# Kernel tuning notes

Measured on AMD Instinct MI355X. Metric: run time of the kernel, lower is better.

Reference implementation:

```python
import jax, jax.numpy as jnp
import numpy as np
import math

S, B, F, D, H, L, DFF, PRED = 448, 64, 8, 256, 8, 4, 256, 96
DK = D // H
EPS = 1e-5


def _pos_enc(length, d_model):
    pos = jnp.arange(length, dtype=jnp.float32)[:, None]            # [S,1]
    div = jnp.exp(jnp.arange(0, d_model, 2, dtype=jnp.float32) * (-math.log(10000.0) / d_model))
    pe = jnp.zeros((length, d_model), jnp.float32)
    pe = pe.at[:, 0::2].set(jnp.sin(pos * div))
    pe = pe.at[:, 1::2].set(jnp.cos(pos * div))
    return pe[:, None, :]                                            # [S,1,D]


def _layernorm(x, g, b):
    mu = jnp.mean(x, axis=-1, keepdims=True)
    var = jnp.mean((x - mu) ** 2, axis=-1, keepdims=True)
    return (x - mu) / jnp.sqrt(var + EPS) * g + b


def setup_inputs() -> dict:
    key = jax.random.key(0)
    ks = jax.random.split(key, 12)
    g = lambda k, shape: (jax.random.normal(k, shape) * 0.02).astype(jnp.float32)
    return {
        "src": jax.random.normal(ks[0], (S, B, F), jnp.float32),
        "w_in": g(ks[1], (F, D)), "b_in": jnp.zeros((D,), jnp.float32),
        "Wq": g(ks[2], (L, D, D)), "bq": jnp.zeros((L, D), jnp.float32),
        "Wk": g(ks[3], (L, D, D)), "bk": jnp.zeros((L, D), jnp.float32),
        "Wv": g(ks[4], (L, D, D)), "bv": jnp.zeros((L, D), jnp.float32),
        "Wo": g(ks[5], (L, D, D)), "bo": jnp.zeros((L, D), jnp.float32),
        "g1": jnp.ones((L, D), jnp.float32), "be1": jnp.zeros((L, D), jnp.float32),
        "W1": g(ks[6], (L, D, DFF)), "b1": jnp.zeros((L, DFF), jnp.float32),
        "W2": g(ks[7], (L, DFF, D)), "b2": jnp.zeros((L, D), jnp.float32),
        "g2": jnp.ones((L, D), jnp.float32), "be2": jnp.zeros((L, D), jnp.float32),
        "w_out": g(ks[8], (D, F)), "b_out": jnp.zeros((F,), jnp.float32),
    }


def reference(src, w_in, b_in, Wq, bq, Wk, bk, Wv, bv, Wo, bo,
              g1, be1, W1, b1, W2, b2, g2, be2, w_out, b_out):
    x = src @ w_in + b_in                 # [S,B,D]
    x = x + _pos_enc(S, D)

    scale = math.sqrt(DK)

    def layer(x, p):
        wq, bq_, wk, bk_, wv, bv_, wo, bo_, g1_, be1_, w1, b1_, w2, b2_, g2_, be2_ = p
        Q = (x @ wq + bq_).reshape(S, B, H, DK)
        K = (x @ wk + bk_).reshape(S, B, H, DK)
        V = (x @ wv + bv_).reshape(S, B, H, DK)
        scores = jnp.einsum("sbhd,tbhd->bhst", Q, K) / scale   # [B,H,S,S]
        attn = jax.nn.softmax(scores, axis=-1)
        ctx = jnp.einsum("bhst,tbhd->sbhd", attn, V).reshape(S, B, D)
        x = _layernorm(x + (ctx @ wo + bo_), g1_, be1_)
        ff = jax.nn.relu(x @ w1 + b1_) @ w2 + b2_
        x = _layernorm(x + ff, g2_, be2_)
        return x, None

    x, _ = jax.lax.scan(layer, x, (Wq, bq, Wk, bk, Wv, bv, Wo, bo,
                                   g1, be1, W1, b1, W2, b2, g2, be2))
    return x[-PRED:] @ w_out + b_out      # [PRED,B,F]
```

## Files before the change

### kernel.cpp

```cpp
#include <hip/hip_runtime.h>
#include <hip/hip_bf16.h>
#include <math.h>

#define S_ 448
#define B_ 64
#define F_ 8
#define D_ 256
#define H_ 8
#define DK_ 32
#define L_ 4
#define PRED_ 96
#define NT_ (S_ * B_)
#define PANEL_ (S_ * DK_)
#define VTP_ (32 * 512)

typedef unsigned short bf16_t;
using bf16x8 = __attribute__((ext_vector_type(8))) short;
using f32x4  = __attribute__((ext_vector_type(4))) float;
using f32x16 = __attribute__((ext_vector_type(16))) float;

__device__ __forceinline__ float b2f(bf16_t b) {
  return __uint_as_float(((unsigned)b) << 16);
}
__device__ __forceinline__ bf16_t f2b(float f) {
  unsigned u = __float_as_uint(f);
  u += 0x7fffu + ((u >> 16) & 1u);
  return (bf16_t)(u >> 16);
}
__device__ __forceinline__ unsigned pk2(float lo, float hi) {
  union { __hip_bfloat162 h; unsigned u; } c;
  c.h = __float22bfloat162_rn(make_float2(lo, hi));
  return c.u;
}

__global__ __launch_bounds__(256) void embed_kernel(
    const float* __restrict__ src, const float* __restrict__ w_in,
    const float* __restrict__ b_in, bf16_t* __restrict__ x) {
  int n = blockIdx.x;
  int d = threadIdx.x;
  const float* srow = src + (size_t)n * F_;
  float acc = b_in[d];
#pragma unroll
  for (int f = 0; f < F_; ++f) acc += srow[f] * w_in[f * D_ + d];
  int s = n / B_;
  int i2 = d & ~1;
  float freq = __expf(-9.210340371976184f * (float)i2 / (float)D_);
  float ang = (float)s * freq;
  float pe = (d & 1) ? cosf(ang) : sinf(ang);
  x[(size_t)n * D_ + d] = f2b(acc + pe);
}

__global__ __launch_bounds__(256) void transpose_w_kernel(
    const float* __restrict__ W, bf16_t* __restrict__ Wt) {
  __shared__ float t[32][33];
  int l = blockIdx.z;
  int k0 = blockIdx.x * 32, n0 = blockIdx.y * 32;
  int x = threadIdx.x, y = threadIdx.y;
  const float* src = W + ((size_t)l * 256 + k0) * 256 + n0;
#pragma unroll
  for (int i = y; i < 32; i += 8) t[i][x] = src[(size_t)i * 256 + x];
  __syncthreads();
  bf16_t* dst = Wt + ((size_t)l * 256 + n0) * 256 + k0;
#pragma unroll
  for (int i = y; i < 32; i += 8) dst[(size_t)i * 256 + x] = f2b(t[x][i]);
}

__global__ __launch_bounds__(512) void vtrans_kernel(
    const bf16_t* __restrict__ V, bf16_t* __restrict__ Vt) {
  __shared__ bf16_t t[32][456];
  int bh = blockIdx.x, tid = threadIdx.x;
  const bf16_t* Vp = V + (size_t)bh * PANEL_;
#pragma unroll
  for (int p = 0; p < 4; ++p) {
    int idx = tid + p * 512;
    if (idx < 1792) {
      int s = idx >> 2, c = idx & 3;
      uint4 v = *(const uint4*)(Vp + s * 32 + c * 8);
      unsigned w[4] = {v.x, v.y, v.z, v.w};
#pragma unroll
      for (int e = 0; e < 8; ++e) {
        bf16_t val = (bf16_t)((e & 1) ? (w[e >> 1] >> 16) : (w[e >> 1] & 0xffff));
        *(bf16_t*)((char*)&t[0][0] + (c * 8 + e) * 912 + s * 2) = val;
      }
    }
  }
  __syncthreads();
  bf16_t* Op = Vt + (size_t)bh * VTP_;
#pragma unroll
  for (int p = 0; p < 4; ++p) {
    int idx = tid + p * 512;
    int dk = idx >> 6, sl = idx & 63;
    uint4 v = {0, 0, 0, 0};
    if (sl < 56) v = *(const uint4*)((char*)&t[0][0] + dk * 912 + sl * 16);
    *(uint4*)(Op + dk * 512 + sl * 8) = v;
  }
}

template <int ALAY, int OLAY, int RELU>
__device__ __forceinline__ void gemm_body(
    const bf16_t* __restrict__ A, const bf16_t* __restrict__ Wt,
    const float* __restrict__ bias, bf16_t* __restrict__ Y, int m0, int n0) {
  __shared__ bf16_t As[2][128][32];
  __shared__ bf16_t Bs[2][128][32];
  int tid = threadIdx.x, lane = tid & 63, wv = tid >> 6;
  int wr = wv >> 2, wc = wv & 3;
  int jg = lane >> 4, fr = lane & 15;
  int s_row = tid >> 2;
  int s_p = tid & 3;

  uint4 rA, rB;

  auto stage_load = [&](int kt) {
    int k0 = kt * 32;
    int ls = s_p ^ ((s_row >> 1) & 3);
    const bf16_t* ap;
    if (ALAY == 0) {
      ap = A + (size_t)(m0 + s_row) * 256 + k0 + ls * 8;
    } else {
      int n = m0 + s_row;
      int k = k0 + ls * 8;
      ap = A + ((size_t)(((n & 63) << 3) | (k >> 5)) * S_ + (n >> 6)) * DK_ +
           (k & 31);
    }
    rA = *(const uint4*)ap;
    rB = *(const uint4*)(Wt + (size_t)(n0 + s_row) * 256 + k0 + ls * 8);
  };
  auto stage_write = [&](int buf) {
    *(uint4*)(&As[buf][s_row][s_p * 8]) = rA;
    *(uint4*)(&Bs[buf][s_row][s_p * 8]) = rB;
  };

  f32x4 zero = {0.f, 0.f, 0.f, 0.f};
  f32x4 acc[4][2];
#pragma unroll
  for (int i = 0; i < 4; ++i)
#pragma unroll
    for (int j = 0; j < 2; ++j) acc[i][j] = zero;

  stage_load(0);
  stage_write(0);
  __syncthreads();

  for (int kt = 0; kt < 8; ++kt) {
    int buf = kt & 1;
    if (kt < 7) stage_load(kt + 1);
    bf16x8 af[4], bfr[2];
#pragma unroll
    for (int mi = 0; mi < 4; ++mi) {
      int row = wr * 64 + mi * 16 + fr;
      af[mi] = *(const bf16x8*)((const char*)&As[buf][0][0] + row * 64 +
                                ((jg ^ ((row >> 1) & 3)) << 4));
    }
#pragma unroll
    for (int ni = 0; ni < 2; ++ni) {
      int rn = wc * 32 + ni * 16 + fr;
      bfr[ni] = *(const bf16x8*)((const char*)&Bs[buf][0][0] + rn * 64 +
                                 ((jg ^ ((rn >> 1) & 3)) << 4));
    }
#pragma unroll
    for (int mi = 0; mi < 4; ++mi)
#pragma unroll
      for (int ni = 0; ni < 2; ++ni)
        acc[mi][ni] = __builtin_amdgcn_mfma_f32_16x16x32_bf16(
            af[mi], bfr[ni], acc[mi][ni], 0, 0, 0);
    if (kt < 7) {
      stage_write((kt + 1) & 1);
      __syncthreads();
    }
  }

  __syncthreads();
  char* ep0 = (char*)&As[0][0][0] + wv * 1024;
  float bcol[2];
#pragma unroll
  for (int ni = 0; ni < 2; ++ni) bcol[ni] = bias[n0 + wc * 32 + ni * 16 + fr];
#pragma unroll
  for (int mi = 0; mi < 4; ++mi) {
    char* ep = ep0 + (mi & 1) * 8192;
#pragma unroll
    for (int ni = 0; ni < 2; ++ni)
#pragma unroll
      for (int r = 0; r < 4; ++r) {
        float v = acc[mi][ni][r] + bcol[ni];
        if (RELU) v = fmaxf(v, 0.f);
        int row = jg * 4 + r;
        int cb = (ni * 16 + fr) * 2;
        *(bf16_t*)(ep + row * 64 + (cb ^ (jg << 4))) = f2b(v);
      }
    int row16 = lane >> 2, c = lane & 3;
    uint4 v = *(uint4*)(ep + row16 * 64 +
                        ((c << 4) ^ (((row16 >> 2) & 3) << 4)));
    int n = m0 + wr * 64 + mi * 16 + row16;
    if (OLAY == 0) {
      *(uint4*)((char*)(Y + (size_t)n * 256 + n0 + wc * 32) + c * 16) = v;
    } else {
      int h = (n0 + wc * 32) >> 5;
      *(uint4*)((char*)(Y + ((size_t)(((n & 63) << 3) | h) * S_ + (n >> 6)) *
                                DK_) +
                c * 16) = v;
    }
  }
}

__global__ __launch_bounds__(512, 4) void gemm_qkv_kernel(
    const bf16_t* __restrict__ A, const bf16_t* __restrict__ wq,
    const bf16_t* __restrict__ wk, const bf16_t* __restrict__ wvp,
    const float* __restrict__ bq, const float* __restrict__ bk,
    const float* __restrict__ bvp, bf16_t* __restrict__ yq,
    bf16_t* __restrict__ yk, bf16_t* __restrict__ yv) {
  int bid = blockIdx.x;
  int w = (bid & 7) * 168 + (bid >> 3);
  int sel = w % 6;
  int m0 = (w / 6) * 128;
  int mtx = sel >> 1;
  const bf16_t* W = mtx == 0 ? wq : mtx == 1 ? wk : wvp;
  const float* bb = mtx == 0 ? bq : mtx == 1 ? bk : bvp;
  bf16_t* Y = mtx == 0 ? yq : mtx == 1 ? yk : yv;
  gemm_body<0, 1, 0>(A, W, bb, Y, m0, (sel & 1) * 128);
}

__global__ __launch_bounds__(512, 4) void gemm_relu_kernel(
    const bf16_t* __restrict__ A, const bf16_t* __restrict__ Wt,
    const float* __restrict__ bias, bf16_t* __restrict__ Y) {
  int bid = blockIdx.x;
  int w = (bid & 7) * 56 + (bid >> 3);
  gemm_body<0, 0, 1>(A, Wt, bias, Y, (w >> 1) * 128, (w & 1) * 128);
}

template <int ALAY>
__global__ __launch_bounds__(512, 2) void gemm_ln_kernel(
    const bf16_t* __restrict__ A, const bf16_t* __restrict__ Wt,
    const float* __restrict__ bias, const float* __restrict__ g,
    const float* __restrict__ be, bf16_t* __restrict__ x) {
  __shared__ char smem[40960];
  int tid = threadIdx.x, lane = tid & 63, wv = tid >> 6;
  int wr = wv >> 2, wc = wv & 3;
  int jg = lane >> 4, fr = lane & 15;
  int bid = blockIdx.x;
  int m0 = ((bid & 7) * 56 + (bid >> 3)) * 64;

  uint4 rA, rB0, rB1;
  auto stage_load = [&](int kt) {
    int k0 = kt * 32;
    if (tid < 256) {
      int row = tid >> 2, p = tid & 3;
      int ls = p ^ ((row >> 1) & 3);
      const bf16_t* ap;
      if (ALAY == 0) {
        ap = A + (size_t)(m0 + row) * 256 + k0 + ls * 8;
      } else {
        int n = m0 + row;
        int k = k0 + ls * 8;
        ap = A + ((size_t)(((n & 63) << 3) | (k >> 5)) * S_ + (n >> 6)) * DK_ +
             (k & 31);
      }
      rA = *(const uint4*)ap;
    }
    int p = tid & 3;
    int r0 = tid >> 2, r1 = 128 + (tid >> 2);
    rB0 = *(const uint4*)(Wt + (size_t)r0 * 256 + k0 + (p ^ ((r0 >> 1) & 3)) * 8);
    rB1 = *(const uint4*)(Wt + (size_t)r1 * 256 + k0 + (p ^ ((r1 >> 1) & 3)) * 8);
  };
  auto stage_write = [&](int buf) {
    if (tid < 256)
      *(uint4*)(smem + buf * 4096 + (tid >> 2) * 64 + (tid & 3) * 16) = rA;
    char* bb = smem + 8192 + buf * 16384;
    *(uint4*)(bb + (tid >> 2) * 64 + (tid & 3) * 16) = rB0;
    *(uint4*)(bb + (128 + (tid >> 2)) * 64 + (tid & 3) * 16) = rB1;
  };

  f32x4 zero = {0.f, 0.f, 0.f, 0.f};
  f32x4 acc[2][4];
#pragma unroll
  for (int i = 0; i < 2; ++i)
#pragma unroll
    for (int j = 0; j < 4; ++j) acc[i][j] = zero;

  stage_load(0);
  stage_write(0);
  __syncthreads();

  for (int kt = 0; kt < 8; ++kt) {
    int buf = kt & 1;
    if (kt < 7) stage_load(kt + 1);
    bf16x8 af[2], bfr[4];
#pragma unroll
    for (int mi = 0; mi < 2; ++mi) {
      int row = wr * 32 + mi * 16 + fr;
      af[mi] = *(const bf16x8*)(smem + buf * 4096 + row * 64 +
                                ((jg ^ ((row >> 1) & 3)) << 4));
    }
#pragma unroll
    for (int ni = 0; ni < 4; ++ni) {
      int rn = wc * 64 + ni * 16 + fr;
      bfr[ni] = *(const bf16x8*)(smem + 8192 + buf * 16384 + rn * 64 +
                                 ((jg ^ ((rn >> 1) & 3)) << 4));
    }
#pragma unroll
    for (int mi = 0; mi < 2; ++mi)
#pragma unroll
      for (int ni = 0; ni < 4; ++ni)
        acc[mi][ni] = __builtin_amdgcn_mfma_f32_16x16x32_bf16(
            af[mi], bfr[ni], acc[mi][ni], 0, 0, 0);
    if (kt < 7) {
      stage_write((kt + 1) & 1);
      __syncthreads();
    }
  }

  __syncthreads();
  float* ssum = (float*)smem;
  float* ssq  = (float*)(smem + 1024);
  float* rowm = (float*)(smem + 2048);
  float* rowr = (float*)(smem + 2304);

  float bcol[4], gv[4], bev[4];
#pragma unroll
  for (int ni = 0; ni < 4; ++ni) {
    int c = wc * 64 + ni * 16 + fr;
    bcol[ni] = bias[c];
    gv[ni] = g[c];
    bev[ni] = be[c];
  }
#pragma unroll
  for (int mi = 0; mi < 2; ++mi)
#pragma unroll
    for (int r = 0; r < 4; ++r) {
      int row = wr * 32 + mi * 16 + jg * 4 + r;
      size_t gbase = (size_t)(m0 + row) * 256 + wc * 64 + fr;
      float s = 0.f, s2 = 0.f;
#pragma unroll
      for (int ni = 0; ni < 4; ++ni) {
        float v = acc[mi][ni][r] + bcol[ni] + b2f(x[gbase + ni * 16]);
        acc[mi][ni][r] = v;
        s += v;
        s2 += v * v;
      }
#pragma unroll
      for (int off = 1; off <= 8; off <<= 1) {
        s += __shfl_xor(s, off);
        s2 += __shfl_xor(s2, off);
      }
      if (fr == 0) {
        ssum[row * 4 + wc] = s;
        ssq[row * 4 + wc] = s2;
      }
    }
  __syncthreads();
  if (tid < 64) {
    float s = ssum[tid * 4] + ssum[tid * 4 + 1] + ssum[tid * 4 + 2] +
              ssum[tid * 4 + 3];
    float q = ssq[tid * 4] + ssq[tid * 4 + 1] + ssq[tid * 4 + 2] +
              ssq[tid * 4 + 3];
    float mean = s * (1.f / 256.f);
    float var = q * (1.f / 256.f) - mean * mean;
    rowm[tid] = mean;
    rowr[tid] = rsqrtf(var + 1e-5f);
  }
  __syncthreads();
  char* ep0 = smem + 8192 + wv * 2048;
#pragma unroll
  for (int mi = 0; mi < 2; ++mi) {
    char* ep = ep0 + mi * 16384;
#pragma unroll
    for (int r = 0; r < 4; ++r) {
      int row = wr * 32 + mi * 16 + jg * 4 + r;
      float mean = rowm[row], rinv = rowr[row];
#pragma unroll
      for (int ni = 0; ni < 4; ++ni) {
        float lnv = (acc[mi][ni][r] - mean) * rinv * gv[ni] + bev[ni];
        int cb = (ni * 16 + fr) * 2;
        *(bf16_t*)(ep + (jg * 4 + r) * 128 + (cb ^ (jg << 4))) = f2b(lnv);
      }
    }
    int row16 = lane >> 2;
#pragma unroll
    for (int ps = 0; ps < 2; ++ps) {
      int ch = (lane & 3) + ps * 4;
      uint4 v = *(uint4*)(ep + row16 * 128 + ((ch * 16) ^ ((row16 >> 2) << 4)));
      *(uint4*)(x + (size_t)(m0 + wr * 32 + mi * 16 + row16) * 256 + wc * 64 +
                ch * 8) = v;
    }
  }
}

__global__ __launch_bounds__(448) void attn_v5_kernel(
    bf16_t* __restrict__ Q, const bf16_t* __restrict__ K,
    const bf16_t* __restrict__ Vt) {
  __shared__ char Ep[7][2560];
  int tid = threadIdx.x, lane = tid & 63, wv = tid >> 6;
  int bid = blockIdx.x;
  int xcd = bid & 7, j = bid >> 3;
  int bh = ((j >> 1) << 3) | xcd;
  int qt = (j & 1) * 7 + wv;
  int q0 = qt * 32;
  bf16_t* Qp = Q + (size_t)bh * PANEL_;
  const bf16_t* Kp = K + (size_t)bh * PANEL_;
  const bf16_t* Vp = Vt + (size_t)bh * VTP_;
  int lo31 = lane & 31, hi = lane >> 5;
  const float sc_c = 0.25503484f;
  const f32x16 z16 = {0.f, 0.f, 0.f, 0.f, 0.f, 0.f, 0.f, 0.f,
                      0.f, 0.f, 0.f, 0.f, 0.f, 0.f, 0.f, 0.f};

  bf16x8 qf0 = *(const bf16x8*)(Qp + (q0 + lo31) * 32 + hi * 8);
  bf16x8 qf1 = *(const bf16x8*)(Qp + (q0 + lo31) * 32 + 16 + hi * 8);

  float m_run = -3.0e38f, l_run = 0.f;
  f32x16 o = z16;

  for (int kc = 0; kc < 7; ++kc) {
    int t0 = kc * 64;
    f32x16 s0 = z16, s1 = z16;
    {
      const bf16_t* kr0 = Kp + (t0 + lo31) * 32 + hi * 8;
      const bf16_t* kr1 = Kp + (t0 + 32 + lo31) * 32 + hi * 8;
      bf16x8 ka0 = *(const bf16x8*)(kr0);
      bf16x8 ka1 = *(const bf16x8*)(kr0 + 16);
      bf16x8 kb0 = *(const bf16x8*)(kr1);
      bf16x8 kb1 = *(const bf16x8*)(kr1 + 16);
      __builtin_amdgcn_s_setprio(1);
      s0 = __builtin_amdgcn_mfma_f32_32x32x16_bf16(ka0, qf0, s0, 0, 0, 0);
      s0 = __builtin_amdgcn_mfma_f32_32x32x16_bf16(ka1, qf1, s0, 0, 0, 0);
      s1 = __builtin_amdgcn_mfma_f32_32x32x16_bf16(kb0, qf0, s1, 0, 0, 0);
      s1 = __builtin_amdgcn_mfma_f32_32x32x16_bf16(kb1, qf1, s1, 0, 0, 0);
      __builtin_amdgcn_s_setprio(0);
    }
    float cm = -3.0e38f;
#pragma unroll
    for (int r = 0; r < 16; ++r) cm = fmaxf(cm, fmaxf(s0[r], s1[r]));
    cm = fmaxf(cm, __shfl_xor(cm, 32));
    if (!__all(cm <= m_run + 16.0f)) {
      float m_new = fmaxf(m_run, cm);
      float scale = exp2f((m_run - m_new) * sc_c);
      l_run *= scale;
#pragma unroll
      for (int r = 0; r < 16; ++r) o[r] *= scale;
      m_run = m_new;
    }
    float ls = 0.f;
#pragma unroll
    for (int r = 0; r < 16; ++r) {
      float p0 = exp2f((s0[r] - m_run) * sc_c);
      float p1 = exp2f((s1[r] - m_run) * sc_c);
      s0[r] = p0; s1[r] = p1;
      ls += p0 + p1;
    }
    ls += __shfl_xor(ls, 32);
    l_run += ls;

#define PV_SUB(SV, RB, TOFF)                                                  \
    {                                                                         \
      unsigned a0 = pk2(SV[RB + 0], SV[RB + 1]);                              \
      unsigned a1 = pk2(SV[RB + 2], SV[RB + 3]);                              \
      unsigned b0 = pk2(SV[RB + 4], SV[RB + 5]);                              \
      unsigned b1 = pk2(SV[RB + 6], SV[RB + 7]);                              \
      unsigned xa0 = (unsigned)__shfl_xor((int)a0, 32);                       \
      unsigned xa1 = (unsigned)__shfl_xor((int)a1, 32);                       \
      unsigned xb0 = (unsigned)__shfl_xor((int)b0, 32);                       \
      unsigned xb1 = (unsigned)__shfl_xor((int)b1, 32);                       \
      union { unsigned u[4]; bf16x8 v; } pf;                                  \
      pf.u[0] = hi ? xb0 : a0;                                                \
      pf.u[1] = hi ? xb1 : a1;                                                \
      pf.u[2] = hi ? b0 : xa0;                                                \
      pf.u[3] = hi ? b1 : xa1;                                                \
      bf16x8 vf = *(const bf16x8*)(Vp + lo31 * 512 + (TOFF) + hi * 8);        \
      o = __builtin_amdgcn_mfma_f32_32x32x16_bf16(pf.v, vf, o, 0, 0, 0);      \
    }
    PV_SUB(s0, 0, t0)
    PV_SUB(s0, 8, t0 + 16)
    PV_SUB(s1, 0, t0 + 32)
    PV_SUB(s1, 8, t0 + 48)
#undef PV_SUB
  }

  float inv = 1.f / l_run;
  char* ep = &Ep[wv][0];
#pragma unroll
  for (int r = 0; r < 16; ++r) {
    int q = (r & 3) + 8 * (r >> 2) + 4 * hi;
    float iq = __shfl(inv, q);
    *(bf16_t*)(ep + q * 80 + lo31 * 2) = f2b(o[r] * iq);
  }
#pragma unroll
  for (int ps = 0; ps < 2; ++ps) {
    int row = ps * 16 + (lane >> 2), ch = lane & 3;
    uint4 v = *(uint4*)(ep + row * 80 + ch * 16);
    *(uint4*)(Qp + (q0 + row) * 32 + ch * 8) = v;
  }
}

__global__ __launch_bounds__(512) void attn_v3f_kernel(
    bf16_t* __restrict__ Q, const bf16_t* __restrict__ K,
    const bf16_t* __restrict__ Vsrc) {
  __shared__ bf16_t Vt[32][520];
  __shared__ char Pbuf[8][2048];
  int tid = threadIdx.x, lane = tid & 63, wv = tid >> 6;
  int bid = blockIdx.x;
  int bh = (bid & 7) | ((bid >> 5) << 3);
  int chunk = (bid >> 3) & 3;
  bf16_t* Qp = Q + (size_t)bh * PANEL_;
  const bf16_t* Kp = K + (size_t)bh * PANEL_;
  int jg = lane >> 4, fr = lane & 15;

  const bf16_t* Vp = Vsrc + (size_t)bh * PANEL_;
  for (int idx = tid; idx < 448 * 4; idx += 512) {
    int t = idx >> 2, c = idx & 3;
    uint4 vv = *(const uint4*)(Vp + t * 32 + c * 8);
    unsigned w[4] = {vv.x, vv.y, vv.z, vv.w};
#pragma unroll
    for (int e = 0; e < 8; ++e) {
      bf16_t val = (bf16_t)((e & 1) ? (w[e >> 1] >> 16) : (w[e >> 1] & 0xffff));
      *(bf16_t*)((char*)&Vt[0][0] + (c * 8 + e) * 1040 + t * 2) = val;
    }
  }
  __syncthreads();

  int q0 = chunk * 128 + wv * 16;
  if (q0 < S_) {
    const float sc_c = 0.25503484f;
    f32x4 zero = {0.f, 0.f, 0.f, 0.f};
    bf16x8 qf = *(const bf16x8*)(Qp + (q0 + fr) * 32 + jg * 8);
    f32x4 s2[28];
#pragma unroll
    for (int ct = 0; ct < 28; ++ct) {
      bf16x8 kf = *(const bf16x8*)(Kp + (ct * 16 + fr) * 32 + jg * 8);
      s2[ct] = __builtin_amdgcn_mfma_f32_16x16x32_bf16(kf, qf, zero, 0, 0, 0);
    }
    float m = s2[0][0];
#pragma unroll
    for (int ct = 0; ct < 28; ++ct)
#pragma unroll
      for (int r = 0; r < 4; ++r) m = fmaxf(m, s2[ct][r]);
    m = fmaxf(m, __shfl_xor(m, 16));
    m = fmaxf(m, __shfl_xor(m, 32));
    float l = 0.f;
#pragma unroll
    for (int ct = 0; ct < 28; ++ct)
#pragma unroll
      for (int r = 0; r < 4; ++r) {
        float p = exp2f((s2[ct][r] - m) * sc_c);
        s2[ct][r] = p;
        l += p;
      }
    l += __shfl_xor(l, 16);
    l += __shfl_xor(l, 32);
    float inv = 1.f / l;

    char* pb0 = &Pbuf[wv][0];
    f32x4 o[2] = {zero, zero};
#pragma unroll
    for (int c = 0; c < 14; ++c) {
      char* pb = pb0 + (c & 1) * 1024;
      uint2 w0, w1;
      w0.x = pk2(s2[2 * c][0], s2[2 * c][1]);
      w0.y = pk2(s2[2 * c][2], s2[2 * c][3]);
      w1.x = pk2(s2[2 * c + 1][0], s2[2 * c + 1][1]);
      w1.y = pk2(s2[2 * c + 1][2], s2[2 * c + 1][3]);
      *(uint2*)(pb + fr * 64 + 8 * jg) = w0;
      *(uint2*)(pb + fr * 64 + 32 + 8 * jg) = w1;
      bf16x8 pf = *(const bf16x8*)(pb + fr * 64 + jg * 16);
#pragma unroll
      for (int nt = 0; nt < 2; ++nt) {
        bf16x8 vf = *(const bf16x8*)((const char*)&Vt[0][0] +
                                     (nt * 16 + fr) * 1040 +
                                     (c * 32 + jg * 8) * 2);
        o[nt] = __builtin_amdgcn_mfma_f32_16x16x32_bf16(pf, vf, o[nt], 0, 0, 0);
      }
    }
    float invq[4];
#pragma unroll
    for (int r = 0; r < 4; ++r) invq[r] = __shfl(inv, jg * 4 + r);
#pragma unroll
    for (int nt = 0; nt < 2; ++nt)
#pragma unroll
      for (int r = 0; r < 4; ++r) {
        float v = o[nt][r] * invq[r];
        int row = jg * 4 + r;
        int cb = (nt * 16 + fr) * 2;
        *(bf16_t*)(pb0 + row * 64 + (cb ^ (jg << 4))) = f2b(v);
      }
    {
      int row16 = lane >> 2, c = lane & 3;
      uint4 v = *(uint4*)(pb0 + row16 * 64 +
                          ((c << 4) ^ (((row16 >> 2) & 3) << 4)));
      *(uint4*)(Qp + (q0 + row16) * 32 + c * 8) = v;
    }
  }
}

__global__ __launch_bounds__(256) void out_kernel(
    const bf16_t* __restrict__ x, const float* __restrict__ w_out,
    const float* __restrict__ b_out, float* __restrict__ out) {
  int idx = blockIdx.x * 256 + threadIdx.x;
  int f = idx & 7;
  int pb = idx >> 3;
  const bf16_t* xrow = x + ((size_t)(S_ - PRED_) * B_ + pb) * D_;
  float acc = b_out[f];
  for (int dd = 0; dd < D_; ++dd) acc += b2f(xrow[dd]) * w_out[dd * F_ + f];
  out[idx] = acc;
}

extern "C" void kernel_launch(void* const* d_in, const int* in_sizes, int n_in,
                              void* d_out, int out_size, void* d_ws, size_t ws_size,
                              hipStream_t stream) {
  const float* src  = (const float*)d_in[0];
  const float* w_in = (const float*)d_in[1];
  const float* b_in = (const float*)d_in[2];
  const float* Wq = (const float*)d_in[3];
  const float* bq = (const float*)d_in[4];
  const float* Wk = (const float*)d_in[5];
  const float* bk = (const float*)d_in[6];
  const float* Wv = (const float*)d_in[7];
  const float* bv = (const float*)d_in[8];
  const float* Wo = (const float*)d_in[9];
  const float* bo = (const float*)d_in[10];
  const float* g1 = (const float*)d_in[11];
  const float* be1 = (const float*)d_in[12];
  const float* W1 = (const float*)d_in[13];
  const float* b1 = (const float*)d_in[14];
  const float* W2 = (const float*)d_in[15];
  const float* b2 = (const float*)d_in[16];
  const float* g2 = (const float*)d_in[17];
  const float* be2 = (const float*)d_in[18];
  const float* w_out = (const float*)d_in[19];
  const float* b_out = (const float*)d_in[20];
  float* out = (float*)d_out;

  const size_t NTD = (size_t)NT_ * D_;
  bf16_t* xb = (bf16_t*)d_ws;
  bf16_t* qb = xb + NTD;
  bf16_t* kb = qb + NTD;
  bf16_t* vb = kb + NTD;
  bf16_t* wt = vb + NTD;
  const size_t WSZ = (size_t)L_ * 65536;
  bf16_t* wtq = wt;
  bf16_t* wtk = wtq + WSZ;
  bf16_t* wtv = wtk + WSZ;
  bf16_t* wto = wtv + WSZ;
  bf16_t* wt1 = wto + WSZ;
  bf16_t* wt2 = wt1 + WSZ;
  bf16_t* vtb = wt2 + WSZ;

  const size_t NEED = ((size_t)4 * NTD + 6 * WSZ + (size_t)512 * VTP_) * 2;
  const int use_vt = (ws_size >= NEED) ? 1 : 0;

  dim3 tb(32, 8), tg(8, 8, L_);
  transpose_w_kernel<<<tg, tb, 0, stream>>>(Wq, wtq);
  transpose_w_kernel<<<tg, tb, 0, stream>>>(Wk, wtk);
  transpose_w_kernel<<<tg, tb, 0, stream>>>(Wv, wtv);
  transpose_w_kernel<<<tg, tb, 0, stream>>>(Wo, wto);
  transpose_w_kernel<<<tg, tb, 0, stream>>>(W1, wt1);
  transpose_w_kernel<<<tg, tb, 0, stream>>>(W2, wt2);

  embed_kernel<<<NT_, 256, 0, stream>>>(src, w_in, b_in, xb);

  for (int l = 0; l < L_; ++l) {
    const size_t woff = (size_t)l * 65536;
    const size_t boff = (size_t)l * D_;
    gemm_qkv_kernel<<<1344, 512, 0, stream>>>(
        xb, wtq + woff, wtk + woff, wtv + woff, bq + boff, bk + boff,
        bv + boff, qb, kb, vb);
    if (use_vt) {
      vtrans_kernel<<<512, 512, 0, stream>>>(vb, vtb);
      attn_v5_kernel<<<1024, 448, 0, stream>>>(qb, kb, vtb);
    } else {
      attn_v3f_kernel<<<2048, 512, 0, stream>>>(qb, kb, vb);
    }
    gemm_ln_kernel<1><<<448, 512, 0, stream>>>(qb, wto + woff, bo + boff,
                                               g1 + boff, be1 + boff, xb);
    gemm_relu_kernel<<<448, 512, 0, stream>>>(xb, wt1 + woff, b1 + boff, qb);
    gemm_ln_kernel<0><<<448, 512, 0, stream>>>(qb, wt2 + woff, b2 + boff,
                                               g2 + boff, be2 + boff, xb);
  }

  out_kernel<<<(PRED_ * B_ * F_) / 256, 256, 0, stream>>>(xb, w_out, b_out, out);
}
```

Baseline: 536.3 us.

## Fold softmax scale into Wq, use direct global-to-LDS loads, two query tiles per wave

Folds the attention softmax scale (1/sqrt(dk)·log2e) into the Q weights and bias so the softmax no longer multiplies every score. The GEMM kernels now stage tiles with global_load_lds straight into shared memory instead of going through registers. The attention kernel gives each wave two 32-row query tiles that share K and V fragment loads, halving the grid to one block per (batch, head). The costs are more live registers per wave in attention, fewer blocks in flight, and a single barrier per k-step in the GEMMs.

```diff
diff --git a/kernel.cpp b/kernel.cpp
--- a/kernel.cpp
+++ b/kernel.cpp
@@ -13,6 +13,7 @@
 #define NT_ (S_ * B_)
 #define PANEL_ (S_ * DK_)
 #define VTP_ (32 * 512)
+#define SCQ_ 0.25503484f
 
 typedef unsigned short bf16_t;
 using bf16x8 = __attribute__((ext_vector_type(8))) short;
@@ -31,6 +32,11 @@
   union { __hip_bfloat162 h; unsigned u; } c;
   c.h = __float22bfloat162_rn(make_float2(lo, hi));
   return c.u;
+}
+__device__ __forceinline__ void gload16(const bf16_t* g, char* l) {
+  __builtin_amdgcn_global_load_lds(
+      (const __attribute__((address_space(1))) unsigned*)g,
+      (__attribute__((address_space(3))) unsigned*)l, 16, 0, 0);
 }
 
 __global__ __launch_bounds__(256) void embed_kernel(
@@ -51,7 +57,7 @@
 }
 
 __global__ __launch_bounds__(256) void transpose_w_kernel(
-    const float* __restrict__ W, bf16_t* __restrict__ Wt) {
+    const float* __restrict__ W, bf16_t* __restrict__ Wt, float scale) {
   __shared__ float t[32][33];
   int l = blockIdx.z;
   int k0 = blockIdx.x * 32, n0 = blockIdx.y * 32;
@@ -62,7 +68,7 @@
   __syncthreads();
   bf16_t* dst = Wt + ((size_t)l * 256 + n0) * 256 + k0;
 #pragma unroll
-  for (int i = y; i < 32; i += 8) dst[(size_t)i * 256 + x] = f2b(t[x][i]);
+  for (int i = y; i < 32; i += 8) dst[(size_t)i * 256 + x] = f2b(t[x][i] * scale);
 }
 
 __global__ __launch_bounds__(512) void vtrans_kernel(
@@ -99,7 +105,8 @@
 template <int ALAY, int OLAY, int RELU>
 __device__ __forceinline__ void gemm_body(
     const bf16_t* __restrict__ A, const bf16_t* __restrict__ Wt,
-    const float* __restrict__ bias, bf16_t* __restrict__ Y, int m0, int n0) {
+    const float* __restrict__ bias, float bscale, bf16_t* __restrict__ Y,
+    int m0, int n0) {
   __shared__ bf16_t As[2][128][32];
   __shared__ bf16_t Bs[2][128][32];
   int tid = threadIdx.x, lane = tid & 63, wv = tid >> 6;
@@ -108,9 +115,7 @@
   int s_row = tid >> 2;
   int s_p = tid & 3;
 
-  uint4 rA, rB;
-
-  auto stage_load = [&](int kt) {
+  auto stage = [&](int kt, int buf) {
     int k0 = kt * 32;
     int ls = s_p ^ ((s_row >> 1) & 3);
     const bf16_t* ap;
@@ -122,12 +127,9 @@
       ap = A + ((size_t)(((n & 63) << 3) | (k >> 5)) * S_ + (n >> 6)) * DK_ +
            (k & 31);
     }
-    rA = *(const uint4*)ap;
-    rB = *(const uint4*)(Wt + (size_t)(n0 + s_row) * 256 + k0 + ls * 8);
-  };
-  auto stage_write = [&](int buf) {
-    *(uint4*)(&As[buf][s_row][s_p * 8]) = rA;
-    *(uint4*)(&Bs[buf][s_row][s_p * 8]) = rB;
+    const bf16_t* bp = Wt + (size_t)(n0 + s_row) * 256 + k0 + ls * 8;
+    gload16(ap, (char*)As + buf * 8192 + wv * 1024);
+    gload16(bp, (char*)Bs + buf * 8192 + wv * 1024);
   };
 
   f32x4 zero = {0.f, 0.f, 0.f, 0.f};
@@ -137,13 +139,12 @@
 #pragma unroll
     for (int j = 0; j < 2; ++j) acc[i][j] = zero;
 
-  stage_load(0);
-  stage_write(0);
+  stage(0, 0);
   __syncthreads();
 
   for (int kt = 0; kt < 8; ++kt) {
     int buf = kt & 1;
-    if (kt < 7) stage_load(kt + 1);
+    if (kt < 7) stage(kt + 1, buf ^ 1);
     bf16x8 af[4], bfr[2];
 #pragma unroll
     for (int mi = 0; mi < 4; ++mi) {
@@ -163,17 +164,14 @@
       for (int ni = 0; ni < 2; ++ni)
         acc[mi][ni] = __builtin_amdgcn_mfma_f32_16x16x32_bf16(
             af[mi], bfr[ni], acc[mi][ni], 0, 0, 0);
-    if (kt < 7) {
-      stage_write((kt + 1) & 1);
-      __syncthreads();
-    }
-  }
-
-  __syncthreads();
+    __syncthreads();
+  }
+
   char* ep0 = (char*)&As[0][0][0] + wv * 1024;
   float bcol[2];
 #pragma unroll
-  for (int ni = 0; ni < 2; ++ni) bcol[ni] = bias[n0 + wc * 32 + ni * 16 + fr];
+  for (int ni = 0; ni < 2; ++ni)
+    bcol[ni] = bias[n0 + wc * 32 + ni * 16 + fr] * bscale;
 #pragma unroll
   for (int mi = 0; mi < 4; ++mi) {
     char* ep = ep0 + (mi & 1) * 8192;
@@ -216,7 +214,8 @@
   const bf16_t* W = mtx == 0 ? wq : mtx == 1 ? wk : wvp;
   const float* bb = mtx == 0 ? bq : mtx == 1 ? bk : bvp;
   bf16_t* Y = mtx == 0 ? yq : mtx == 1 ? yk : yv;
-  gemm_body<0, 1, 0>(A, W, bb, Y, m0, (sel & 1) * 128);
+  float bscale = mtx == 0 ? SCQ_ : 1.0f;
+  gemm_body<0, 1, 0>(A, W, bb, bscale, Y, m0, (sel & 1) * 128);
 }
 
 __global__ __launch_bounds__(512, 4) void gemm_relu_kernel(
@@ -224,7 +223,7 @@
     const float* __restrict__ bias, bf16_t* __restrict__ Y) {
   int bid = blockIdx.x;
   int w = (bid & 7) * 56 + (bid >> 3);
-  gemm_body<0, 0, 1>(A, Wt, bias, Y, (w >> 1) * 128, (w & 1) * 128);
+  gemm_body<0, 0, 1>(A, Wt, bias, 1.0f, Y, (w >> 1) * 128, (w & 1) * 128);
 }
 
 template <int ALAY>
@@ -239,8 +238,7 @@
   int bid = blockIdx.x;
   int m0 = ((bid & 7) * 56 + (bid >> 3)) * 64;
 
-  uint4 rA, rB0, rB1;
-  auto stage_load = [&](int kt) {
+  auto stage = [&](int kt, int buf) {
     int k0 = kt * 32;
     if (tid < 256) {
       int row = tid >> 2, p = tid & 3;
@@ -254,19 +252,14 @@
         ap = A + ((size_t)(((n & 63) << 3) | (k >> 5)) * S_ + (n >> 6)) * DK_ +
              (k & 31);
       }
-      rA = *(const uint4*)ap;
+      gload16(ap, smem + buf * 4096 + wv * 1024);
     }
     int p = tid & 3;
     int r0 = tid >> 2, r1 = 128 + (tid >> 2);
-    rB0 = *(const uint4*)(Wt + (size_t)r0 * 256 + k0 + (p ^ ((r0 >> 1) & 3)) * 8);
-    rB1 = *(const uint4*)(Wt + (size_t)r1 * 256 + k0 + (p ^ ((r1 >> 1) & 3)) * 8);
-  };
-  auto stage_write = [&](int buf) {
-    if (tid < 256)
-      *(uint4*)(smem + buf * 4096 + (tid >> 2) * 64 + (tid & 3) * 16) = rA;
-    char* bb = smem + 8192 + buf * 16384;
-    *(uint4*)(bb + (tid >> 2) * 64 + (tid & 3) * 16) = rB0;
-    *(uint4*)(bb + (128 + (tid >> 2)) * 64 + (tid & 3) * 16) = rB1;
+    gload16(Wt + (size_t)r0 * 256 + k0 + (p ^ ((r0 >> 1) & 3)) * 8,
+            smem + 8192 + buf * 16384 + wv * 1024);
+    gload16(Wt + (size_t)r1 * 256 + k0 + (p ^ ((r1 >> 1) & 3)) * 8,
+            smem + 8192 + buf * 16384 + 8192 + wv * 1024);
   };
 
   f32x4 zero = {0.f, 0.f, 0.f, 0.f};
@@ -276,13 +269,12 @@
 #pragma unroll
     for (int j = 0; j < 4; ++j) acc[i][j] = zero;
 
-  stage_load(0);
-  stage_write(0);
+  stage(0, 0);
   __syncthreads();
 
   for (int kt = 0; kt < 8; ++kt) {
     int buf = kt & 1;
-    if (kt < 7) stage_load(kt + 1);
+    if (kt < 7) stage(kt + 1, buf ^ 1);
     bf16x8 af[2], bfr[4];
 #pragma unroll
     for (int mi = 0; mi < 2; ++mi) {
@@ -302,13 +294,9 @@
       for (int ni = 0; ni < 4; ++ni)
         acc[mi][ni] = __builtin_amdgcn_mfma_f32_16x16x32_bf16(
             af[mi], bfr[ni], acc[mi][ni], 0, 0, 0);
-    if (kt < 7) {
-      stage_write((kt + 1) & 1);
-      __syncthreads();
-    }
-  }
-
-  __syncthreads();
+    __syncthreads();
+  }
+
   float* ssum = (float*)smem;
   float* ssq  = (float*)(smem + 1024);
   float* rowm = (float*)(smem + 2048);
@@ -384,108 +372,132 @@
   }
 }
 
-__global__ __launch_bounds__(448) void attn_v5_kernel(
+__global__ __launch_bounds__(448) void attn_v6_kernel(
     bf16_t* __restrict__ Q, const bf16_t* __restrict__ K,
     const bf16_t* __restrict__ Vt) {
   __shared__ char Ep[7][2560];
   int tid = threadIdx.x, lane = tid & 63, wv = tid >> 6;
-  int bid = blockIdx.x;
-  int xcd = bid & 7, j = bid >> 3;
-  int bh = ((j >> 1) << 3) | xcd;
-  int qt = (j & 1) * 7 + wv;
-  int q0 = qt * 32;
+  int bh = blockIdx.x;
   bf16_t* Qp = Q + (size_t)bh * PANEL_;
   const bf16_t* Kp = K + (size_t)bh * PANEL_;
   const bf16_t* Vp = Vt + (size_t)bh * VTP_;
   int lo31 = lane & 31, hi = lane >> 5;
-  const float sc_c = 0.25503484f;
   const f32x16 z16 = {0.f, 0.f, 0.f, 0.f, 0.f, 0.f, 0.f, 0.f,
                       0.f, 0.f, 0.f, 0.f, 0.f, 0.f, 0.f, 0.f};
-
-  bf16x8 qf0 = *(const bf16x8*)(Qp + (q0 + lo31) * 32 + hi * 8);
-  bf16x8 qf1 = *(const bf16x8*)(Qp + (q0 + lo31) * 32 + 16 + hi * 8);
-
-  float m_run = -3.0e38f, l_run = 0.f;
-  f32x16 o = z16;
-
-  for (int kc = 0; kc < 7; ++kc) {
-    int t0 = kc * 64;
-    f32x16 s0 = z16, s1 = z16;
+  int q0a = wv * 32, q0b = q0a + 224;
+
+  bf16x8 qa0 = *(const bf16x8*)(Qp + (q0a + lo31) * 32 + hi * 8);
+  bf16x8 qa1 = *(const bf16x8*)(Qp + (q0a + lo31) * 32 + 16 + hi * 8);
+  bf16x8 qb0 = *(const bf16x8*)(Qp + (q0b + lo31) * 32 + hi * 8);
+  bf16x8 qb1 = *(const bf16x8*)(Qp + (q0b + lo31) * 32 + 16 + hi * 8);
+
+  float mA = -3.0e38f, lA = 0.f, mB = -3.0e38f, lB = 0.f;
+  f32x16 oA = z16, oB = z16;
+
+#define PV_SUB(SV, RB, TOFF, OD)                                              \
+  {                                                                           \
+    unsigned a0 = pk2(SV[RB + 0], SV[RB + 1]);                                \
+    unsigned a1 = pk2(SV[RB + 2], SV[RB + 3]);                                \
+    unsigned b0 = pk2(SV[RB + 4], SV[RB + 5]);                                \
+    unsigned b1 = pk2(SV[RB + 6], SV[RB + 7]);                                \
+    unsigned xa0 = (unsigned)__shfl_xor((int)a0, 32);                         \
+    unsigned xa1 = (unsigned)__shfl_xor((int)a1, 32);                         \
+    unsigned xb0 = (unsigned)__shfl_xor((int)b0, 32);                         \
+    unsigned xb1 = (unsigned)__shfl_xor((int)b1, 32);                         \
+    union { unsigned u[4]; bf16x8 v; } pf;                                    \
+    pf.u[0] = hi ? xb0 : a0;                                                  \
+    pf.u[1] = hi ? xb1 : a1;                                                  \
+    pf.u[2] = hi ? b0 : xa0;                                                  \
+    pf.u[3] = hi ? b1 : xa1;                                                  \
+    bf16x8 vf = *(const bf16x8*)(Vp + lo31 * 512 + (TOFF) + hi * 8);          \
+    OD = __builtin_amdgcn_mfma_f32_32x32x16_bf16(pf.v, vf, OD, 0, 0, 0);      \
+  }
+
+  for (int kc = 0; kc < 14; ++kc) {
+    int t0 = kc * 32;
+    const bf16_t* kr = Kp + (t0 + lo31) * 32 + hi * 8;
+    bf16x8 k0 = *(const bf16x8*)(kr);
+    bf16x8 k1 = *(const bf16x8*)(kr + 16);
+    f32x16 sA = z16, sB = z16;
+    __builtin_amdgcn_s_setprio(1);
+    sA = __builtin_amdgcn_mfma_f32_32x32x16_bf16(k0, qa0, sA, 0, 0, 0);
+    sA = __builtin_amdgcn_mfma_f32_32x32x16_bf16(k1, qa1, sA, 0, 0, 0);
+    sB = __builtin_amdgcn_mfma_f32_32x32x16_bf16(k0, qb0, sB, 0, 0, 0);
+    sB = __builtin_amdgcn_mfma_f32_32x32x16_bf16(k1, qb1, sB, 0, 0, 0);
+    __builtin_amdgcn_s_setprio(0);
+
     {
-      const bf16_t* kr0 = Kp + (t0 + lo31) * 32 + hi * 8;
-      const bf16_t* kr1 = Kp + (t0 + 32 + lo31) * 32 + hi * 8;
-      bf16x8 ka0 = *(const bf16x8*)(kr0);
-      bf16x8 ka1 = *(const bf16x8*)(kr0 + 16);
-      bf16x8 kb0 = *(const bf16x8*)(kr1);
-      bf16x8 kb1 = *(const bf16x8*)(kr1 + 16);
-      __builtin_amdgcn_s_setprio(1);
-      s0 = __builtin_amdgcn_mfma_f32_32x32x16_bf16(ka0, qf0, s0, 0, 0, 0);
-      s0 = __builtin_amdgcn_mfma_f32_32x32x16_bf16(ka1, qf1, s0, 0, 0, 0);
-      s1 = __builtin_amdgcn_mfma_f32_32x32x16_bf16(kb0, qf0, s1, 0, 0, 0);
-      s1 = __builtin_amdgcn_mfma_f32_32x32x16_bf16(kb1, qf1, s1, 0, 0, 0);
-      __builtin_amdgcn_s_setprio(0);
-    }
-    float cm = -3.0e38f;
-#pragma unroll
-    for (int r = 0; r < 16; ++r) cm = fmaxf(cm, fmaxf(s0[r], s1[r]));
-    cm = fmaxf(cm, __shfl_xor(cm, 32));
-    if (!__all(cm <= m_run + 16.0f)) {
-      float m_new = fmaxf(m_run, cm);
-      float scale = exp2f((m_run - m_new) * sc_c);
-      l_run *= scale;
-#pragma unroll
-      for (int r = 0; r < 16; ++r) o[r] *= scale;
-      m_run = m_new;
-    }
-    float ls = 0.f;
+      float cm = -3.0e38f;
+#pragma unroll
+      for (int r = 0; r < 16; ++r) cm = fmaxf(cm, sA[r]);
+      cm = fmaxf(cm, __shfl_xor(cm, 32));
+      if (!__all(cm <= mA + 8.0f)) {
+        float mn = fmaxf(mA, cm);
+        float sc = exp2f(mA - mn);
+        lA *= sc;
+#pragma unroll
+        for (int r = 0; r < 16; ++r) oA[r] *= sc;
+        mA = mn;
+      }
+      float ls = 0.f;
+#pragma unroll
+      for (int r = 0; r < 16; ++r) {
+        float p = exp2f(sA[r] - mA);
+        sA[r] = p;
+        ls += p;
+      }
+      ls += __shfl_xor(ls, 32);
+      lA += ls;
+    }
+    {
+      float cm = -3.0e38f;
+#pragma unroll
+      for (int r = 0; r < 16; ++r) cm = fmaxf(cm, sB[r]);
+      cm = fmaxf(cm, __shfl_xor(cm, 32));
+      if (!__all(cm <= mB + 8.0f)) {
+        float mn = fmaxf(mB, cm);
+        float sc = exp2f(mB - mn);
+        lB *= sc;
+#pragma unroll
+        for (int r = 0; r < 16; ++r) oB[r] *= sc;
+        mB = mn;
+      }
+      float ls = 0.f;
+#pragma unroll
+      for (int r = 0; r < 16; ++r) {
+        float p = exp2f(sB[r] - mB);
+        sB[r] = p;
+        ls += p;
+      }
+      ls += __shfl_xor(ls, 32);
+      lB += ls;
+    }
+    PV_SUB(sA, 0, t0, oA)
+    PV_SUB(sA, 8, t0 + 16, oA)
+    PV_SUB(sB, 0, t0, oB)
+    PV_SUB(sB, 8, t0 + 16, oB)
+  }
+#undef PV_SUB
+
+  char* ep = &Ep[wv][0];
+#pragma unroll
+  for (int tt = 0; tt < 2; ++tt) {
+    float l_run = tt ? lB : lA;
+    int q0 = tt ? q0b : q0a;
+    float inv = 1.f / l_run;
 #pragma unroll
     for (int r = 0; r < 16; ++r) {
-      float p0 = exp2f((s0[r] - m_run) * sc_c);
-      float p1 = exp2f((s1[r] - m_run) * sc_c);
-      s0[r] = p0; s1[r] = p1;
-      ls += p0 + p1;
-    }
-    ls += __shfl_xor(ls, 32);
-    l_run += ls;
-
-#define PV_SUB(SV, RB, TOFF)                                                  \
-    {                                                                         \
-      unsigned a0 = pk2(SV[RB + 0], SV[RB + 1]);                              \
-      unsigned a1 = pk2(SV[RB + 2], SV[RB + 3]);                              \
-      unsigned b0 = pk2(SV[RB + 4], SV[RB + 5]);                              \
-      unsigned b1 = pk2(SV[RB + 6], SV[RB + 7]);                              \
-      unsigned xa0 = (unsigned)__shfl_xor((int)a0, 32);                       \
-      unsigned xa1 = (unsigned)__shfl_xor((int)a1, 32);                       \
-      unsigned xb0 = (unsigned)__shfl_xor((int)b0, 32);                       \
-      unsigned xb1 = (unsigned)__shfl_xor((int)b1, 32);                       \
-      union { unsigned u[4]; bf16x8 v; } pf;                                  \
-      pf.u[0] = hi ? xb0 : a0;                                                \
-      pf.u[1] = hi ? xb1 : a1;                                                \
-      pf.u[2] = hi ? b0 : xa0;                                                \
-      pf.u[3] = hi ? b1 : xa1;                                                \
-      bf16x8 vf = *(const bf16x8*)(Vp + lo31 * 512 + (TOFF) + hi * 8);        \
-      o = __builtin_amdgcn_mfma_f32_32x32x16_bf16(pf.v, vf, o, 0, 0, 0);      \
-    }
-    PV_SUB(s0, 0, t0)
-    PV_SUB(s0, 8, t0 + 16)
-    PV_SUB(s1, 0, t0 + 32)
-    PV_SUB(s1, 8, t0 + 48)
-#undef PV_SUB
-  }
-
-  float inv = 1.f / l_run;
-  char* ep = &Ep[wv][0];
-#pragma unroll
-  for (int r = 0; r < 16; ++r) {
-    int q = (r & 3) + 8 * (r >> 2) + 4 * hi;
-    float iq = __shfl(inv, q);
-    *(bf16_t*)(ep + q * 80 + lo31 * 2) = f2b(o[r] * iq);
-  }
-#pragma unroll
-  for (int ps = 0; ps < 2; ++ps) {
-    int row = ps * 16 + (lane >> 2), ch = lane & 3;
-    uint4 v = *(uint4*)(ep + row * 80 + ch * 16);
-    *(uint4*)(Qp + (q0 + row) * 32 + ch * 8) = v;
+      int q = (r & 3) + 8 * (r >> 2) + 4 * hi;
+      float iq = __shfl(inv, q);
+      float ov = tt ? oB[r] : oA[r];
+      *(bf16_t*)(ep + q * 80 + lo31 * 2) = f2b(ov * iq);
+    }
+#pragma unroll
+    for (int ps = 0; ps < 2; ++ps) {
+      int row = ps * 16 + (lane >> 2), ch = lane & 3;
+      uint4 v = *(uint4*)(ep + row * 80 + ch * 16);
+      *(uint4*)(Qp + (q0 + row) * 32 + ch * 8) = v;
+    }
   }
 }
 
@@ -517,7 +529,6 @@
 
   int q0 = chunk * 128 + wv * 16;
   if (q0 < S_) {
-    const float sc_c = 0.25503484f;
     f32x4 zero = {0.f, 0.f, 0.f, 0.f};
     bf16x8 qf = *(const bf16x8*)(Qp + (q0 + fr) * 32 + jg * 8);
     f32x4 s2[28];
@@ -538,7 +549,7 @@
     for (int ct = 0; ct < 28; ++ct)
 #pragma unroll
       for (int r = 0; r < 4; ++r) {
-        float p = exp2f((s2[ct][r] - m) * sc_c);
+        float p = exp2f(s2[ct][r] - m);
         s2[ct][r] = p;
         l += p;
       }
@@ -645,12 +656,12 @@
   const int use_vt = (ws_size >= NEED) ? 1 : 0;
 
   dim3 tb(32, 8), tg(8, 8, L_);
-  transpose_w_kernel<<<tg, tb, 0, stream>>>(Wq, wtq);
-  transpose_w_kernel<<<tg, tb, 0, stream>>>(Wk, wtk);
-  transpose_w_kernel<<<tg, tb, 0, stream>>>(Wv, wtv);
-  transpose_w_kernel<<<tg, tb, 0, stream>>>(Wo, wto);
-  transpose_w_kernel<<<tg, tb, 0, stream>>>(W1, wt1);
-  transpose_w_kernel<<<tg, tb, 0, stream>>>(W2, wt2);
+  transpose_w_kernel<<<tg, tb, 0, stream>>>(Wq, wtq, SCQ_);
+  transpose_w_kernel<<<tg, tb, 0, stream>>>(Wk, wtk, 1.0f);
+  transpose_w_kernel<<<tg, tb, 0, stream>>>(Wv, wtv, 1.0f);
+  transpose_w_kernel<<<tg, tb, 0, stream>>>(Wo, wto, 1.0f);
+  transpose_w_kernel<<<tg, tb, 0, stream>>>(W1, wt1, 1.0f);
+  transpose_w_kernel<<<tg, tb, 0, stream>>>(W2, wt2, 1.0f);
 
   embed_kernel<<<NT_, 256, 0, stream>>>(src, w_in, b_in, xb);
 
@@ -662,7 +673,7 @@
         bv + boff, qb, kb, vb);
     if (use_vt) {
       vtrans_kernel<<<512, 512, 0, stream>>>(vb, vtb);
-      attn_v5_kernel<<<1024, 448, 0, stream>>>(qb, kb, vtb);
+      attn_v6_kernel<<<512, 448, 0, stream>>>(qb, kb, vtb);
     } else {
       attn_v3f_kernel<<<2048, 512, 0, stream>>>(qb, kb, vb);
     }
```

New measurement: 525.8 us. No clear change (-2.0%).
